# Optimization experiments

Measured on AMD Instinct MI355X. Metric: run time of the kernel, lower is better.

Reference implementation:

```python
import jax, jax.numpy as jnp
import numpy as np
import math

HEAD_SIZE = 128
N_EMBED = 2048
B, T = 4, 4096
TOP_K_RATIO = 0.1


def setup_inputs() -> dict:
    key = jax.random.key(0)
    k1, k2, k3, k4 = jax.random.split(key, 4)
    index = jax.random.normal(k1, (B, T, N_EMBED), dtype=jnp.float32)
    s = 1.0 / math.sqrt(N_EMBED)
    Wq = jax.random.normal(k2, (N_EMBED, HEAD_SIZE), dtype=jnp.float32) * s
    Wk = jax.random.normal(k3, (N_EMBED, HEAD_SIZE), dtype=jnp.float32) * s
    Wv = jax.random.normal(k4, (N_EMBED, HEAD_SIZE), dtype=jnp.float32) * s
    return {"index": index, "Wq": Wq, "Wk": Wk, "Wv": Wv}


def reference(index, Wq, Wk, Wv):
    # memory = index (self-attention case)
    Bv, Tv, _ = index.shape
    top_k = int(TOP_K_RATIO * Tv)  # 409

    q = index @ Wq  # [B, T, D]
    k = index @ Wk
    v = index @ Wv

    q_norms = jnp.linalg.norm(q, axis=-1)  # [B, T]
    _, top_idx = jax.lax.top_k(q_norms, top_k)  # [B, K]

    idx = top_idx[..., None]  # [B, K, 1]
    q_topk = jnp.take_along_axis(q, idx, axis=1)  # [B, K, D]
    k_topk = jnp.take_along_axis(k, idx, axis=1)
    v_topk = jnp.take_along_axis(v, idx, axis=1)

    w = jnp.einsum('bid,bjd->bij', q_topk, k_topk) / math.sqrt(HEAD_SIZE)
    # eval mode: no causal mask (only applied in training), dropout = identity
    w = jax.nn.softmax(w, axis=-1)  # stable softmax (internal max subtraction)
    out_topk = w @ v_topk  # [B, K, D]

    batch_idx = jnp.arange(Bv)[:, None]  # [B, 1]
    output = jnp.zeros((Bv, Tv, HEAD_SIZE), dtype=out_topk.dtype)
    output = output.at[batch_idx, top_idx].add(out_topk)  # scatter_add (indices unique)
    return output
```

## Files before the change

### kernel.cpp

```cpp
#include <hip/hip_runtime.h>
#include <hip/hip_bf16.h>

#define NB 4
#define NT 4096
#define NC 2048
#define ND 128
#define NK 409
#define KPAD 416
#define NM (NB * NK)

typedef __attribute__((ext_vector_type(8))) short short8;
typedef __attribute__((ext_vector_type(4))) float f32x4;

union S8U { short8 v; ushort u[8]; };

__device__ __forceinline__ void split2(float x, ushort& h, ushort& l) {
    union { float f; unsigned u; } a; a.f = x;
    unsigned r = a.u + 0x7FFFu + ((a.u >> 16) & 1u);
    h = (ushort)(r >> 16);
    union { unsigned u; float f; } hb; hb.u = ((unsigned)h) << 16;
    float res = x - hb.f;
    union { float f; unsigned u; } b; b.f = res;
    unsigned r2 = b.u + 0x7FFFu + ((b.u >> 16) & 1u);
    l = (ushort)(r2 >> 16);
}

__device__ __forceinline__ uint4 pack8(const ushort* s) {
    uint4 v;
    v.x = (unsigned)s[0] | ((unsigned)s[1] << 16);
    v.y = (unsigned)s[2] | ((unsigned)s[3] << 16);
    v.z = (unsigned)s[4] | ((unsigned)s[5] << 16);
    v.w = (unsigned)s[6] | ((unsigned)s[7] << 16);
    return v;
}

__device__ __forceinline__ int slotOf(int n, int lq) {
    return n * 4 + ((lq + (n >> 1)) & 3);
}

__device__ __forceinline__ void gll16(const void* g, void* l) {
    __builtin_amdgcn_global_load_lds(
        (const __attribute__((address_space(1))) unsigned*)g,
        (__attribute__((address_space(3))) unsigned*)l, 16, 0, 0);
}

__global__ __launch_bounds__(256) void bconv_tiles(
    const float* __restrict__ W, ushort* __restrict__ Bt)
{
    const int kt = blockIdx.x;
    const int t = threadIdx.x;
    const int n = t & 127;
    const int lq0 = (t >> 7) * 2;
    #pragma unroll
    for (int e = 0; e < 2; ++e) {
        int lq = lq0 + e;
        ushort h[8], l[8];
        #pragma unroll
        for (int j = 0; j < 8; ++j) {
            float x = W[(size_t)(kt * 32 + lq * 8 + j) * ND + n];
            split2(x, h[j], l[j]);
        }
        int slot = slotOf(n, lq);
        *(uint4*)&Bt[((size_t)(kt * 2 + 0) * 512 + slot) * 8] = pack8(h);
        *(uint4*)&Bt[((size_t)(kt * 2 + 1) * 512 + slot) * 8] = pack8(l);
    }
}

__global__ __launch_bounds__(256) void qgemm_v2(
    const float* __restrict__ A, const ushort* __restrict__ Bt,
    float* __restrict__ q1, float* __restrict__ q2)
{
    __shared__ __align__(16) ushort BS[2][2][4096];

    const int tid = threadIdx.x;
    const int w = tid >> 6, lane = tid & 63;
    const int wm = w >> 1, wn = w & 1;
    const int lrow = lane & 15, lq = lane >> 4;
    const int m0 = blockIdx.x * 128;
    const int kb = blockIdx.y * (NC / 2);
    const int kt0 = blockIdx.y * ((NC / 2) / 32);
    const int KITER = (NC / 2) / 32;

    const float* arow[4];
    #pragma unroll
    for (int mi = 0; mi < 4; ++mi)
        arow[mi] = A + (size_t)(m0 + wm * 64 + mi * 16 + lrow) * NC + kb + lq * 8;

    int boff[4];
    #pragma unroll
    for (int ni = 0; ni < 4; ++ni)
        boff[ni] = slotOf(wn * 64 + ni * 16 + lrow, lq) * 8;

    f32x4 acc[4][4];
    #pragma unroll
    for (int i = 0; i < 4; ++i)
        #pragma unroll
        for (int j = 0; j < 4; ++j) acc[i][j] = (f32x4){0.f, 0.f, 0.f, 0.f};

    {
        const ushort* gt = Bt + (size_t)kt0 * 2 * 512 * 8;
        #pragma unroll
        for (int p = 0; p < 2; ++p)
            #pragma unroll
            for (int c2 = 0; c2 < 2; ++c2) {
                int c = 2 * w + c2;
                gll16(gt + ((size_t)p * 512 + c * 64 + lane) * 8,
                      &BS[0][p][(c * 64) * 8]);
            }
    }
    float4 fa[8];
    #pragma unroll
    for (int mi = 0; mi < 4; ++mi) {
        fa[2 * mi + 0] = *(const float4*)(arow[mi] + 0);
        fa[2 * mi + 1] = *(const float4*)(arow[mi] + 4);
    }
    __syncthreads();

    for (int kt = 0; kt < KITER; ++kt) {
        const int buf = kt & 1;
        if (kt + 1 < KITER) {
            const ushort* gt = Bt + (size_t)(kt0 + kt + 1) * 2 * 512 * 8;
            #pragma unroll
            for (int p = 0; p < 2; ++p)
                #pragma unroll
                for (int c2 = 0; c2 < 2; ++c2) {
                    int c = 2 * w + c2;
                    gll16(gt + ((size_t)p * 512 + c * 64 + lane) * 8,
                          &BS[buf ^ 1][p][(c * 64) * 8]);
                }
        }
        short8 ah[4], al[4];
        #pragma unroll
        for (int mi = 0; mi < 4; ++mi) {
            S8U H, L;
            float xs[8] = {fa[2*mi].x, fa[2*mi].y, fa[2*mi].z, fa[2*mi].w,
                           fa[2*mi+1].x, fa[2*mi+1].y, fa[2*mi+1].z, fa[2*mi+1].w};
            #pragma unroll
            for (int j = 0; j < 8; ++j) split2(xs[j], H.u[j], L.u[j]);
            ah[mi] = H.v; al[mi] = L.v;
        }
        if (kt + 1 < KITER) {
            #pragma unroll
            for (int mi = 0; mi < 4; ++mi) {
                fa[2 * mi + 0] = *(const float4*)(arow[mi] + (kt + 1) * 32);
                fa[2 * mi + 1] = *(const float4*)(arow[mi] + (kt + 1) * 32 + 4);
            }
        }
        #pragma unroll
        for (int ni = 0; ni < 4; ++ni) {
            short8 bh = *(const short8*)&BS[buf][0][boff[ni]];
            short8 bl = *(const short8*)&BS[buf][1][boff[ni]];
            #pragma unroll
            for (int mi = 0; mi < 4; ++mi) {
                acc[mi][ni] = __builtin_amdgcn_mfma_f32_16x16x32_bf16(ah[mi], bh, acc[mi][ni], 0, 0, 0);
                acc[mi][ni] = __builtin_amdgcn_mfma_f32_16x16x32_bf16(ah[mi], bl, acc[mi][ni], 0, 0, 0);
                acc[mi][ni] = __builtin_amdgcn_mfma_f32_16x16x32_bf16(al[mi], bh, acc[mi][ni], 0, 0, 0);
            }
        }
        __syncthreads();
    }

    float* __restrict__ qd = blockIdx.y ? q2 : q1;
    #pragma unroll
    for (int ni = 0; ni < 4; ++ni) {
        const int col = wn * 64 + ni * 16 + lrow;
        #pragma unroll
        for (int mi = 0; mi < 4; ++mi)
            #pragma unroll
            for (int r = 0; r < 4; ++r) {
                const int grow = m0 + wm * 64 + mi * 16 + lq * 4 + r;
                qd[(size_t)grow * ND + col] = acc[mi][ni][r];
            }
    }
}

__global__ __launch_bounds__(256) void kvgemm_v2(
    const float* __restrict__ X, const ushort* __restrict__ Bkt,
    const ushort* __restrict__ Bvt, const int* __restrict__ topi,
    float* __restrict__ ktop, float* __restrict__ vtop)
{
    __shared__ __align__(16) ushort BS[2][2][4096];

    const int tid = threadIdx.x;
    const int w = tid >> 6, lane = tid & 63;
    const int wm = w >> 1, wn = w & 1;
    const int lrow = lane & 15, lq = lane >> 4;
    const int m0 = blockIdx.x * 64;
    const int kb = blockIdx.y * (NC / 2);
    const int kt0 = blockIdx.y * ((NC / 2) / 32);
    const ushort* __restrict__ Bt = blockIdx.z ? Bvt : Bkt;
    const int KITER = (NC / 2) / 32;

    const float* arow[2];
    #pragma unroll
    for (int mi = 0; mi < 2; ++mi) {
        int gi = m0 + wm * 32 + mi * 16 + lrow;
        int giC = gi < NM ? gi : NM - 1;
        int b = giC / NK, ii = giC % NK;
        int src = topi[b * KPAD + ii];
        arow[mi] = X + ((size_t)b * NT + src) * NC + kb + lq * 8;
    }
    int boff[4];
    #pragma unroll
    for (int ni = 0; ni < 4; ++ni)
        boff[ni] = slotOf(wn * 64 + ni * 16 + lrow, lq) * 8;

    f32x4 acc[2][4];
    #pragma unroll
    for (int i = 0; i < 2; ++i)
        #pragma unroll
        for (int j = 0; j < 4; ++j) acc[i][j] = (f32x4){0.f, 0.f, 0.f, 0.f};

    {
        const ushort* gt = Bt + (size_t)kt0 * 2 * 512 * 8;
        #pragma unroll
        for (int p = 0; p < 2; ++p)
            #pragma unroll
            for (int c2 = 0; c2 < 2; ++c2) {
                int c = 2 * w + c2;
                gll16(gt + ((size_t)p * 512 + c * 64 + lane) * 8,
                      &BS[0][p][(c * 64) * 8]);
            }
    }
    float4 fa[4];
    #pragma unroll
    for (int mi = 0; mi < 2; ++mi) {
        fa[2 * mi + 0] = *(const float4*)(arow[mi] + 0);
        fa[2 * mi + 1] = *(const float4*)(arow[mi] + 4);
    }
    __syncthreads();

    for (int kt = 0; kt < KITER; ++kt) {
        const int buf = kt & 1;
        if (kt + 1 < KITER) {
            const ushort* gt = Bt + (size_t)(kt0 + kt + 1) * 2 * 512 * 8;
            #pragma unroll
            for (int p = 0; p < 2; ++p)
                #pragma unroll
                for (int c2 = 0; c2 < 2; ++c2) {
                    int c = 2 * w + c2;
                    gll16(gt + ((size_t)p * 512 + c * 64 + lane) * 8,
                          &BS[buf ^ 1][p][(c * 64) * 8]);
                }
        }
        short8 ah[2], al[2];
        #pragma unroll
        for (int mi = 0; mi < 2; ++mi) {
            S8U H, L;
            float xs[8] = {fa[2*mi].x, fa[2*mi].y, fa[2*mi].z, fa[2*mi].w,
                           fa[2*mi+1].x, fa[2*mi+1].y, fa[2*mi+1].z, fa[2*mi+1].w};
            #pragma unroll
            for (int j = 0; j < 8; ++j) split2(xs[j], H.u[j], L.u[j]);
            ah[mi] = H.v; al[mi] = L.v;
        }
        if (kt + 1 < KITER) {
            #pragma unroll
            for (int mi = 0; mi < 2; ++mi) {
                fa[2 * mi + 0] = *(const float4*)(arow[mi] + (kt + 1) * 32);
                fa[2 * mi + 1] = *(const float4*)(arow[mi] + (kt + 1) * 32 + 4);
            }
        }
        #pragma unroll
        for (int ni = 0; ni < 4; ++ni) {
            short8 bh = *(const short8*)&BS[buf][0][boff[ni]];
            short8 bl = *(const short8*)&BS[buf][1][boff[ni]];
            #pragma unroll
            for (int mi = 0; mi < 2; ++mi) {
                acc[mi][ni] = __builtin_amdgcn_mfma_f32_16x16x32_bf16(ah[mi], bh, acc[mi][ni], 0, 0, 0);
                acc[mi][ni] = __builtin_amdgcn_mfma_f32_16x16x32_bf16(ah[mi], bl, acc[mi][ni], 0, 0, 0);
                acc[mi][ni] = __builtin_amdgcn_mfma_f32_16x16x32_bf16(al[mi], bh, acc[mi][ni], 0, 0, 0);
            }
        }
        __syncthreads();
    }

    float* __restrict__ dst = blockIdx.z ? vtop : ktop;
    #pragma unroll
    for (int ni = 0; ni < 4; ++ni) {
        const int col = wn * 64 + ni * 16 + lrow;
        #pragma unroll
        for (int mi = 0; mi < 2; ++mi)
            #pragma unroll
            for (int r = 0; r < 4; ++r) {
                const int grow = m0 + wm * 32 + mi * 16 + lq * 4 + r;
                if (grow < NM)
                    atomicAdd(&dst[(size_t)grow * ND + col], acc[mi][ni][r]);
            }
    }
}

__global__ __launch_bounds__(256) void qnorm_kernel(
    float* __restrict__ q1, const float* __restrict__ q2, float* __restrict__ qn)
{
    const int wv = (blockIdx.x * 256 + threadIdx.x) >> 6;
    const int lane = threadIdx.x & 63;
    float* r1 = q1 + (size_t)wv * ND;
    const float* r2 = q2 + (size_t)wv * ND;
    float a = r1[lane] + r2[lane];
    float b = r1[lane + 64] + r2[lane + 64];
    r1[lane] = a;
    r1[lane + 64] = b;
    float s = a * a + b * b;
    #pragma unroll
    for (int off = 32; off > 0; off >>= 1) s += __shfl_xor(s, off);
    if (lane == 0) qn[wv] = sqrtf(s);
}

__global__ __launch_bounds__(256) void topk_kernel(
    const float* __restrict__ qn, int* __restrict__ topi, int* __restrict__ cnt)
{
    __shared__ int rs[4][64];
    const int b = blockIdx.y;
    const int is = threadIdx.x & 63;
    const int i = blockIdx.x * 64 + is;
    const int chunk = threadIdx.x >> 6;
    const float vi = qn[(size_t)b * NT + i];
    const float4* qv = (const float4*)(qn + (size_t)b * NT + chunk * 1024);
    int rank = 0;
    #pragma unroll 4
    for (int j4 = 0; j4 < 256; ++j4) {
        float4 v = qv[j4];
        int j = chunk * 1024 + j4 * 4;
        rank += (v.x > vi || (v.x == vi && (j + 0) < i)) ? 1 : 0;
        rank += (v.y > vi || (v.y == vi && (j + 1) < i)) ? 1 : 0;
        rank += (v.z > vi || (v.z == vi && (j + 2) < i)) ? 1 : 0;
        rank += (v.w > vi || (v.w == vi && (j + 3) < i)) ? 1 : 0;
    }
    rs[chunk][is] = rank;
    __syncthreads();
    if (threadIdx.x < 64) {
        int rk = rs[0][threadIdx.x] + rs[1][threadIdx.x] + rs[2][threadIdx.x] + rs[3][threadIdx.x];
        if (rk < NK) {
            int p = atomicAdd(&cnt[b], 1);
            topi[b * KPAD + p] = blockIdx.x * 64 + threadIdx.x;
        }
    }
}

__global__ __launch_bounds__(256) void attn_kernel(
    const float* __restrict__ q, const float* __restrict__ ktop,
    const float* __restrict__ vtop, const int* __restrict__ topi,
    float* __restrict__ out)
{
    __shared__ float qs[ND];
    __shared__ float ss[KPAD];
    __shared__ float red[256];
    __shared__ float pv[2][ND];
    const int bi = blockIdx.x;
    const int b = bi / NK, i = bi % NK;
    const int t = threadIdx.x;
    const int row = topi[b * KPAD + i];
    if (t < ND) qs[t] = q[((size_t)b * NT + row) * ND + t];
    __syncthreads();

    const float scale = 0.08838834764831844f;
    float mymax = -1e30f;
    #pragma unroll
    for (int rep = 0; rep < 2; ++rep) {
        int j = t + rep * 256;
        if (j < NK) {
            const float4* kr = (const float4*)(ktop + ((size_t)b * NK + j) * ND);
            const float4* q4 = (const float4*)qs;
            float s = 0.f;
            #pragma unroll
            for (int dd = 0; dd < 32; ++dd) {
                float4 a = q4[dd], kv = kr[dd];
                s += a.x * kv.x + a.y * kv.y + a.z * kv.z + a.w * kv.w;
            }
            s *= scale;
            ss[j] = s;
            mymax = fmaxf(mymax, s);
        }
    }
    red[t] = mymax;
    __syncthreads();
    for (int off = 128; off > 0; off >>= 1) {
        if (t < off) red[t] = fmaxf(red[t], red[t + off]);
        __syncthreads();
    }
    const float mx = red[0];
    __syncthreads();

    float mysum = 0.f;
    #pragma unroll
    for (int rep = 0; rep < 2; ++rep) {
        int j = t + rep * 256;
        if (j < NK) {
            float p = __expf(ss[j] - mx);
            ss[j] = p;
            mysum += p;
        }
    }
    red[t] = mysum;
    __syncthreads();
    for (int off = 128; off > 0; off >>= 1) {
        if (t < off) red[t] += red[t + off];
        __syncthreads();
    }
    const float inv = 1.f / red[0];

    const int col = t & (ND - 1), half = t >> 7;
    float o = 0.f;
    #pragma unroll 4
    for (int j = half; j < NK; j += 2)
        o = fmaf(ss[j], vtop[((size_t)b * NK + j) * ND + col], o);
    pv[half][col] = o;
    __syncthreads();
    if (t < ND)
        out[((size_t)b * NT + row) * ND + t] = (pv[0][t] + pv[1][t]) * inv;
}

extern "C" void kernel_launch(void* const* d_in, const int* in_sizes, int n_in,
                              void* d_out, int out_size, void* d_ws, size_t ws_size,
                              hipStream_t stream)
{
    const float* index = (const float*)d_in[0];
    const float* Wq = (const float*)d_in[1];
    const float* Wk = (const float*)d_in[2];
    const float* Wv = (const float*)d_in[3];
    float* out = (float*)d_out;

    char* ws = (char*)d_ws;
    float*  q1   = (float*)(ws);
    float*  qn   = (float*)(ws + 8388608);
    int*    topi = (int*)  (ws + 8454144);
    int*    cnt  = (int*)  (ws + 8462336);
    ushort* Bqt  = (ushort*)(ws + 8462592);
    float*  ktop = (float*)(ws + 8462592);
    float*  vtop = (float*)(ws + 9300224);

    float*  q2  = (float*)d_out;
    ushort* Bkt = (ushort*)d_out;
    ushort* Bvt = (ushort*)((char*)d_out + 1048576);

    hipMemsetAsync(cnt, 0, NB * sizeof(int), stream);

    bconv_tiles<<<dim3(64), dim3(256), 0, stream>>>(Wq, Bqt);
    qgemm_v2<<<dim3(NB * NT / 128, 2), dim3(256), 0, stream>>>(index, Bqt, q1, q2);
    qnorm_kernel<<<dim3(NB * NT / 4), dim3(256), 0, stream>>>(q1, q2, qn);
    topk_kernel<<<dim3(NT / 64, NB), dim3(256), 0, stream>>>(qn, topi, cnt);
    bconv_tiles<<<dim3(64), dim3(256), 0, stream>>>(Wk, Bkt);
    bconv_tiles<<<dim3(64), dim3(256), 0, stream>>>(Wv, Bvt);
    hipMemsetAsync(ktop, 0, 2 * 837632, stream);
    kvgemm_v2<<<dim3((NM + 63) / 64, 2, 2), dim3(256), 0, stream>>>(
        index, Bkt, Bvt, topi, ktop, vtop);
    hipMemsetAsync(d_out, 0, (size_t)out_size * sizeof(float), stream);
    attn_kernel<<<dim3(NM), dim3(256), 0, stream>>>(q1, ktop, vtop, topi, out);
}
```

Before: 392.2 us.

## Raise split-K to 8 for Q and KV GEMMs using atomic accumulation

The Q projection GEMM now splits the reduction dimension eight ways instead of two, and its partial results are accumulated with atomicAdd into one zeroed buffer instead of two separate buffers that qnorm used to sum. The KV GEMM split also goes from two to eight, and both kernels get a min-blocks-per-CU launch bound. The aim is many more blocks for better CU occupancy on the large Q GEMM. The cost is more fp32 atomic traffic, an extra memset of the Q buffer, and results whose summation order is no longer deterministic.

```diff
diff --git a/kernel.cpp b/kernel.cpp
--- a/kernel.cpp
+++ b/kernel.cpp
@@ -66,9 +66,10 @@
     }
 }
 
-__global__ __launch_bounds__(256) void qgemm_v2(
+#define QSPLIT 8
+__global__ __launch_bounds__(256, 4) void qgemm_v3(
     const float* __restrict__ A, const ushort* __restrict__ Bt,
-    float* __restrict__ q1, float* __restrict__ q2)
+    float* __restrict__ q)
 {
     __shared__ __align__(16) ushort BS[2][2][4096];
 
@@ -77,9 +78,9 @@
     const int wm = w >> 1, wn = w & 1;
     const int lrow = lane & 15, lq = lane >> 4;
     const int m0 = blockIdx.x * 128;
-    const int kb = blockIdx.y * (NC / 2);
-    const int kt0 = blockIdx.y * ((NC / 2) / 32);
-    const int KITER = (NC / 2) / 32;
+    const int kb = blockIdx.y * (NC / QSPLIT);
+    const int kt0 = blockIdx.y * ((NC / QSPLIT) / 32);
+    const int KITER = (NC / QSPLIT) / 32;
 
     const float* arow[4];
     #pragma unroll
@@ -160,7 +161,6 @@
         __syncthreads();
     }
 
-    float* __restrict__ qd = blockIdx.y ? q2 : q1;
     #pragma unroll
     for (int ni = 0; ni < 4; ++ni) {
         const int col = wn * 64 + ni * 16 + lrow;
@@ -169,12 +169,13 @@
             #pragma unroll
             for (int r = 0; r < 4; ++r) {
                 const int grow = m0 + wm * 64 + mi * 16 + lq * 4 + r;
-                qd[(size_t)grow * ND + col] = acc[mi][ni][r];
-            }
-    }
-}
-
-__global__ __launch_bounds__(256) void kvgemm_v2(
+                atomicAdd(&q[(size_t)grow * ND + col], acc[mi][ni][r]);
+            }
+    }
+}
+
+#define KVSPLIT 8
+__global__ __launch_bounds__(256, 4) void kvgemm_v3(
     const float* __restrict__ X, const ushort* __restrict__ Bkt,
     const ushort* __restrict__ Bvt, const int* __restrict__ topi,
     float* __restrict__ ktop, float* __restrict__ vtop)
@@ -186,10 +187,10 @@
     const int wm = w >> 1, wn = w & 1;
     const int lrow = lane & 15, lq = lane >> 4;
     const int m0 = blockIdx.x * 64;
-    const int kb = blockIdx.y * (NC / 2);
-    const int kt0 = blockIdx.y * ((NC / 2) / 32);
+    const int kb = blockIdx.y * (NC / KVSPLIT);
+    const int kt0 = blockIdx.y * ((NC / KVSPLIT) / 32);
     const ushort* __restrict__ Bt = blockIdx.z ? Bvt : Bkt;
-    const int KITER = (NC / 2) / 32;
+    const int KITER = (NC / KVSPLIT) / 32;
 
     const float* arow[2];
     #pragma unroll
@@ -290,16 +291,13 @@
 }
 
 __global__ __launch_bounds__(256) void qnorm_kernel(
-    float* __restrict__ q1, const float* __restrict__ q2, float* __restrict__ qn)
+    const float* __restrict__ q, float* __restrict__ qn)
 {
     const int wv = (blockIdx.x * 256 + threadIdx.x) >> 6;
     const int lane = threadIdx.x & 63;
-    float* r1 = q1 + (size_t)wv * ND;
-    const float* r2 = q2 + (size_t)wv * ND;
-    float a = r1[lane] + r2[lane];
-    float b = r1[lane + 64] + r2[lane + 64];
-    r1[lane] = a;
-    r1[lane + 64] = b;
+    const float* r1 = q + (size_t)wv * ND;
+    float a = r1[lane];
+    float b = r1[lane + 64];
     float s = a * a + b * b;
     #pragma unroll
     for (int off = 32; off > 0; off >>= 1) s += __shfl_xor(s, off);
@@ -429,20 +427,20 @@
     float*  ktop = (float*)(ws + 8462592);
     float*  vtop = (float*)(ws + 9300224);
 
-    float*  q2  = (float*)d_out;
     ushort* Bkt = (ushort*)d_out;
     ushort* Bvt = (ushort*)((char*)d_out + 1048576);
 
     hipMemsetAsync(cnt, 0, NB * sizeof(int), stream);
+    hipMemsetAsync(q1, 0, 8388608, stream);
 
     bconv_tiles<<<dim3(64), dim3(256), 0, stream>>>(Wq, Bqt);
-    qgemm_v2<<<dim3(NB * NT / 128, 2), dim3(256), 0, stream>>>(index, Bqt, q1, q2);
-    qnorm_kernel<<<dim3(NB * NT / 4), dim3(256), 0, stream>>>(q1, q2, qn);
+    qgemm_v3<<<dim3(NB * NT / 128, QSPLIT), dim3(256), 0, stream>>>(index, Bqt, q1);
+    qnorm_kernel<<<dim3(NB * NT / 4), dim3(256), 0, stream>>>(q1, qn);
     topk_kernel<<<dim3(NT / 64, NB), dim3(256), 0, stream>>>(qn, topi, cnt);
     bconv_tiles<<<dim3(64), dim3(256), 0, stream>>>(Wk, Bkt);
     bconv_tiles<<<dim3(64), dim3(256), 0, stream>>>(Wv, Bvt);
     hipMemsetAsync(ktop, 0, 2 * 837632, stream);
-    kvgemm_v2<<<dim3((NM + 63) / 64, 2, 2), dim3(256), 0, stream>>>(
+    kvgemm_v3<<<dim3((NM + 63) / 64, KVSPLIT, 2), dim3(256), 0, stream>>>(
         index, Bkt, Bvt, topi, ktop, vtop);
     hipMemsetAsync(d_out, 0, (size_t)out_size * sizeof(float), stream);
     attn_kernel<<<dim3(NM), dim3(256), 0, stream>>>(q1, ktop, vtop, topi, out);
```

Result: slower. 546.0 us (+39.2%).

## Drop LDS staging in Q/KV GEMMs, load B fragments to registers, raise KV split-K

Applied to the files above, without the earlier changes.

Rewrites the Q and KV projection GEMMs so each wave owns 16 rows across all 128 columns and loads the pre-split bf16 weight fragments straight from global memory into double-buffered registers. This removes shared-memory staging and the per-iteration barriers. The Q tile shrinks to 64 rows, and the KV GEMM split-K grows from 2 to 8 slices to give the small gathered GEMM more blocks. In exchange, weight fragments are re-read from global/L2 by every wave and register pressure rises, and the larger split adds more atomic traffic into ktop/vtop.

```diff
diff --git a/kernel.cpp b/kernel.cpp
--- a/kernel.cpp
+++ b/kernel.cpp
@@ -38,12 +38,6 @@
     return n * 4 + ((lq + (n >> 1)) & 3);
 }
 
-__device__ __forceinline__ void gll16(const void* g, void* l) {
-    __builtin_amdgcn_global_load_lds(
-        (const __attribute__((address_space(1))) unsigned*)g,
-        (__attribute__((address_space(3))) unsigned*)l, 16, 0, 0);
-}
-
 __global__ __launch_bounds__(256) void bconv_tiles(
     const float* __restrict__ W, ushort* __restrict__ Bt)
 {
@@ -66,226 +60,174 @@
     }
 }
 
-__global__ __launch_bounds__(256) void qgemm_v2(
+#define QSPLIT 2
+__global__ __launch_bounds__(256) void qgemm_v5(
     const float* __restrict__ A, const ushort* __restrict__ Bt,
     float* __restrict__ q1, float* __restrict__ q2)
 {
-    __shared__ __align__(16) ushort BS[2][2][4096];
-
     const int tid = threadIdx.x;
     const int w = tid >> 6, lane = tid & 63;
-    const int wm = w >> 1, wn = w & 1;
     const int lrow = lane & 15, lq = lane >> 4;
-    const int m0 = blockIdx.x * 128;
-    const int kb = blockIdx.y * (NC / 2);
-    const int kt0 = blockIdx.y * ((NC / 2) / 32);
-    const int KITER = (NC / 2) / 32;
-
-    const float* arow[4];
-    #pragma unroll
-    for (int mi = 0; mi < 4; ++mi)
-        arow[mi] = A + (size_t)(m0 + wm * 64 + mi * 16 + lrow) * NC + kb + lq * 8;
-
-    int boff[4];
-    #pragma unroll
-    for (int ni = 0; ni < 4; ++ni)
-        boff[ni] = slotOf(wn * 64 + ni * 16 + lrow, lq) * 8;
-
-    f32x4 acc[4][4];
-    #pragma unroll
-    for (int i = 0; i < 4; ++i)
-        #pragma unroll
-        for (int j = 0; j < 4; ++j) acc[i][j] = (f32x4){0.f, 0.f, 0.f, 0.f};
-
+    const int m0 = blockIdx.x * 64;
+    const int KITER = (NC / QSPLIT) / 32;
+    const int kt0 = blockIdx.y * KITER;
+    const int kb = blockIdx.y * (NC / QSPLIT);
+
+    const float* arow = A + (size_t)(m0 + w * 16 + lrow) * NC + kb + lq * 8;
+
+    int boff[8];
+    #pragma unroll
+    for (int ni = 0; ni < 8; ++ni)
+        boff[ni] = slotOf(ni * 16 + lrow, lq) * 8;
+
+    f32x4 acc[8];
+    #pragma unroll
+    for (int i = 0; i < 8; ++i) acc[i] = (f32x4){0.f, 0.f, 0.f, 0.f};
+
+    short8 bhA[8], blA[8], bhB[8], blB[8];
     {
-        const ushort* gt = Bt + (size_t)kt0 * 2 * 512 * 8;
-        #pragma unroll
-        for (int p = 0; p < 2; ++p)
-            #pragma unroll
-            for (int c2 = 0; c2 < 2; ++c2) {
-                int c = 2 * w + c2;
-                gll16(gt + ((size_t)p * 512 + c * 64 + lane) * 8,
-                      &BS[0][p][(c * 64) * 8]);
-            }
-    }
-    float4 fa[8];
-    #pragma unroll
-    for (int mi = 0; mi < 4; ++mi) {
-        fa[2 * mi + 0] = *(const float4*)(arow[mi] + 0);
-        fa[2 * mi + 1] = *(const float4*)(arow[mi] + 4);
-    }
-    __syncthreads();
-
-    for (int kt = 0; kt < KITER; ++kt) {
-        const int buf = kt & 1;
-        if (kt + 1 < KITER) {
-            const ushort* gt = Bt + (size_t)(kt0 + kt + 1) * 2 * 512 * 8;
-            #pragma unroll
-            for (int p = 0; p < 2; ++p)
-                #pragma unroll
-                for (int c2 = 0; c2 < 2; ++c2) {
-                    int c = 2 * w + c2;
-                    gll16(gt + ((size_t)p * 512 + c * 64 + lane) * 8,
-                          &BS[buf ^ 1][p][(c * 64) * 8]);
-                }
-        }
-        short8 ah[4], al[4];
-        #pragma unroll
-        for (int mi = 0; mi < 4; ++mi) {
-            S8U H, L;
-            float xs[8] = {fa[2*mi].x, fa[2*mi].y, fa[2*mi].z, fa[2*mi].w,
-                           fa[2*mi+1].x, fa[2*mi+1].y, fa[2*mi+1].z, fa[2*mi+1].w};
-            #pragma unroll
-            for (int j = 0; j < 8; ++j) split2(xs[j], H.u[j], L.u[j]);
-            ah[mi] = H.v; al[mi] = L.v;
-        }
-        if (kt + 1 < KITER) {
-            #pragma unroll
-            for (int mi = 0; mi < 4; ++mi) {
-                fa[2 * mi + 0] = *(const float4*)(arow[mi] + (kt + 1) * 32);
-                fa[2 * mi + 1] = *(const float4*)(arow[mi] + (kt + 1) * 32 + 4);
-            }
-        }
-        #pragma unroll
-        for (int ni = 0; ni < 4; ++ni) {
-            short8 bh = *(const short8*)&BS[buf][0][boff[ni]];
-            short8 bl = *(const short8*)&BS[buf][1][boff[ni]];
-            #pragma unroll
-            for (int mi = 0; mi < 4; ++mi) {
-                acc[mi][ni] = __builtin_amdgcn_mfma_f32_16x16x32_bf16(ah[mi], bh, acc[mi][ni], 0, 0, 0);
-                acc[mi][ni] = __builtin_amdgcn_mfma_f32_16x16x32_bf16(ah[mi], bl, acc[mi][ni], 0, 0, 0);
-                acc[mi][ni] = __builtin_amdgcn_mfma_f32_16x16x32_bf16(al[mi], bh, acc[mi][ni], 0, 0, 0);
-            }
-        }
-        __syncthreads();
-    }
+        const ushort* gb = Bt + (size_t)kt0 * 8192;
+        #pragma unroll
+        for (int ni = 0; ni < 8; ++ni) {
+            bhA[ni] = *(const short8*)(gb + boff[ni]);
+            blA[ni] = *(const short8*)(gb + 4096 + boff[ni]);
+        }
+    }
+    float4 fa0 = *(const float4*)(arow + 0);
+    float4 fa1 = *(const float4*)(arow + 4);
+
+#define QSTEP(BHC, BLC, BHN, BLN, KT)                                         \
+    {                                                                         \
+        short8 ah, al;                                                        \
+        {                                                                     \
+            S8U H, L;                                                         \
+            float xs[8] = {fa0.x, fa0.y, fa0.z, fa0.w,                        \
+                           fa1.x, fa1.y, fa1.z, fa1.w};                       \
+            _Pragma("unroll")                                                 \
+            for (int j = 0; j < 8; ++j) split2(xs[j], H.u[j], L.u[j]);        \
+            ah = H.v; al = L.v;                                               \
+        }                                                                     \
+        const int ktn = ((KT) + 1 < KITER) ? (KT) + 1 : (KT);                 \
+        const ushort* gbn = Bt + (size_t)(kt0 + ktn) * 8192;                  \
+        _Pragma("unroll")                                                     \
+        for (int ni = 0; ni < 8; ++ni) {                                      \
+            BHN[ni] = *(const short8*)(gbn + boff[ni]);                       \
+            BLN[ni] = *(const short8*)(gbn + 4096 + boff[ni]);                \
+        }                                                                     \
+        fa0 = *(const float4*)(arow + ktn * 32);                              \
+        fa1 = *(const float4*)(arow + ktn * 32 + 4);                          \
+        _Pragma("unroll")                                                     \
+        for (int ni = 0; ni < 8; ++ni) {                                      \
+            acc[ni] = __builtin_amdgcn_mfma_f32_16x16x32_bf16(ah, BHC[ni], acc[ni], 0, 0, 0); \
+            acc[ni] = __builtin_amdgcn_mfma_f32_16x16x32_bf16(ah, BLC[ni], acc[ni], 0, 0, 0); \
+            acc[ni] = __builtin_amdgcn_mfma_f32_16x16x32_bf16(al, BHC[ni], acc[ni], 0, 0, 0); \
+        }                                                                     \
+    }
+
+    for (int kt = 0; kt < KITER; kt += 2) {
+        QSTEP(bhA, blA, bhB, blB, kt);
+        QSTEP(bhB, blB, bhA, blA, kt + 1);
+    }
+#undef QSTEP
 
     float* __restrict__ qd = blockIdx.y ? q2 : q1;
     #pragma unroll
-    for (int ni = 0; ni < 4; ++ni) {
-        const int col = wn * 64 + ni * 16 + lrow;
-        #pragma unroll
-        for (int mi = 0; mi < 4; ++mi)
-            #pragma unroll
-            for (int r = 0; r < 4; ++r) {
-                const int grow = m0 + wm * 64 + mi * 16 + lq * 4 + r;
-                qd[(size_t)grow * ND + col] = acc[mi][ni][r];
-            }
-    }
-}
-
-__global__ __launch_bounds__(256) void kvgemm_v2(
+    for (int ni = 0; ni < 8; ++ni) {
+        const int col = ni * 16 + lrow;
+        #pragma unroll
+        for (int r = 0; r < 4; ++r) {
+            const int grow = m0 + w * 16 + lq * 4 + r;
+            qd[(size_t)grow * ND + col] = acc[ni][r];
+        }
+    }
+}
+
+#define KVSPLIT 8
+__global__ __launch_bounds__(256) void kvgemm_v5(
     const float* __restrict__ X, const ushort* __restrict__ Bkt,
     const ushort* __restrict__ Bvt, const int* __restrict__ topi,
     float* __restrict__ ktop, float* __restrict__ vtop)
 {
-    __shared__ __align__(16) ushort BS[2][2][4096];
-
     const int tid = threadIdx.x;
     const int w = tid >> 6, lane = tid & 63;
-    const int wm = w >> 1, wn = w & 1;
     const int lrow = lane & 15, lq = lane >> 4;
     const int m0 = blockIdx.x * 64;
-    const int kb = blockIdx.y * (NC / 2);
-    const int kt0 = blockIdx.y * ((NC / 2) / 32);
+    const int KITER = (NC / KVSPLIT) / 32;
+    const int kt0 = blockIdx.y * KITER;
+    const int kb = blockIdx.y * (NC / KVSPLIT);
     const ushort* __restrict__ Bt = blockIdx.z ? Bvt : Bkt;
-    const int KITER = (NC / 2) / 32;
-
-    const float* arow[2];
-    #pragma unroll
-    for (int mi = 0; mi < 2; ++mi) {
-        int gi = m0 + wm * 32 + mi * 16 + lrow;
-        int giC = gi < NM ? gi : NM - 1;
-        int b = giC / NK, ii = giC % NK;
-        int src = topi[b * KPAD + ii];
-        arow[mi] = X + ((size_t)b * NT + src) * NC + kb + lq * 8;
-    }
-    int boff[4];
-    #pragma unroll
-    for (int ni = 0; ni < 4; ++ni)
-        boff[ni] = slotOf(wn * 64 + ni * 16 + lrow, lq) * 8;
-
-    f32x4 acc[2][4];
-    #pragma unroll
-    for (int i = 0; i < 2; ++i)
-        #pragma unroll
-        for (int j = 0; j < 4; ++j) acc[i][j] = (f32x4){0.f, 0.f, 0.f, 0.f};
-
+
+    const int gi = m0 + w * 16 + lrow;
+    const int giC = gi < NM ? gi : NM - 1;
+    const int b = giC / NK, ii = giC % NK;
+    const int src = topi[b * KPAD + ii];
+    const float* arow = X + ((size_t)b * NT + src) * NC + kb + lq * 8;
+
+    int boff[8];
+    #pragma unroll
+    for (int ni = 0; ni < 8; ++ni)
+        boff[ni] = slotOf(ni * 16 + lrow, lq) * 8;
+
+    f32x4 acc[8];
+    #pragma unroll
+    for (int i = 0; i < 8; ++i) acc[i] = (f32x4){0.f, 0.f, 0.f, 0.f};
+
+    short8 bhA[8], blA[8], bhB[8], blB[8];
     {
-        const ushort* gt = Bt + (size_t)kt0 * 2 * 512 * 8;
-        #pragma unroll
-        for (int p = 0; p < 2; ++p)
-            #pragma unroll
-            for (int c2 = 0; c2 < 2; ++c2) {
-                int c = 2 * w + c2;
-                gll16(gt + ((size_t)p * 512 + c * 64 + lane) * 8,
-                      &BS[0][p][(c * 64) * 8]);
-            }
-    }
-    float4 fa[4];
-    #pragma unroll
-    for (int mi = 0; mi < 2; ++mi) {
-        fa[2 * mi + 0] = *(const float4*)(arow[mi] + 0);
-        fa[2 * mi + 1] = *(const float4*)(arow[mi] + 4);
-    }
-    __syncthreads();
-
-    for (int kt = 0; kt < KITER; ++kt) {
-        const int buf = kt & 1;
-        if (kt + 1 < KITER) {
-            const ushort* gt = Bt + (size_t)(kt0 + kt + 1) * 2 * 512 * 8;
-            #pragma unroll
-            for (int p = 0; p < 2; ++p)
-                #pragma unroll
-                for (int c2 = 0; c2 < 2; ++c2) {
-                    int c = 2 * w + c2;
-                    gll16(gt + ((size_t)p * 512 + c * 64 + lane) * 8,
-                          &BS[buf ^ 1][p][(c * 64) * 8]);
-                }
-        }
-        short8 ah[2], al[2];
-        #pragma unroll
-        for (int mi = 0; mi < 2; ++mi) {
-            S8U H, L;
-            float xs[8] = {fa[2*mi].x, fa[2*mi].y, fa[2*mi].z, fa[2*mi].w,
-                           fa[2*mi+1].x, fa[2*mi+1].y, fa[2*mi+1].z, fa[2*mi+1].w};
-            #pragma unroll
-            for (int j = 0; j < 8; ++j) split2(xs[j], H.u[j], L.u[j]);
-            ah[mi] = H.v; al[mi] = L.v;
-        }
-        if (kt + 1 < KITER) {
-            #pragma unroll
-            for (int mi = 0; mi < 2; ++mi) {
-                fa[2 * mi + 0] = *(const float4*)(arow[mi] + (kt + 1) * 32);
-                fa[2 * mi + 1] = *(const float4*)(arow[mi] + (kt + 1) * 32 + 4);
-            }
-        }
-        #pragma unroll
-        for (int ni = 0; ni < 4; ++ni) {
-            short8 bh = *(const short8*)&BS[buf][0][boff[ni]];
-            short8 bl = *(const short8*)&BS[buf][1][boff[ni]];
-            #pragma unroll
-            for (int mi = 0; mi < 2; ++mi) {
-                acc[mi][ni] = __builtin_amdgcn_mfma_f32_16x16x32_bf16(ah[mi], bh, acc[mi][ni], 0, 0, 0);
-                acc[mi][ni] = __builtin_amdgcn_mfma_f32_16x16x32_bf16(ah[mi], bl, acc[mi][ni], 0, 0, 0);
-                acc[mi][ni] = __builtin_amdgcn_mfma_f32_16x16x32_bf16(al[mi], bh, acc[mi][ni], 0, 0, 0);
-            }
-        }
-        __syncthreads();
-    }
+        const ushort* gb = Bt + (size_t)kt0 * 8192;
+        #pragma unroll
+        for (int ni = 0; ni < 8; ++ni) {
+            bhA[ni] = *(const short8*)(gb + boff[ni]);
+            blA[ni] = *(const short8*)(gb + 4096 + boff[ni]);
+        }
+    }
+    float4 fa0 = *(const float4*)(arow + 0);
+    float4 fa1 = *(const float4*)(arow + 4);
+
+#define QSTEP(BHC, BLC, BHN, BLN, KT)                                         \
+    {                                                                         \
+        short8 ah, al;                                                        \
+        {                                                                     \
+            S8U H, L;                                                         \
+            float xs[8] = {fa0.x, fa0.y, fa0.z, fa0.w,                        \
+                           fa1.x, fa1.y, fa1.z, fa1.w};                       \
+            _Pragma("unroll")                                                 \
+            for (int j = 0; j < 8; ++j) split2(xs[j], H.u[j], L.u[j]);        \
+            ah = H.v; al = L.v;                                               \
+        }                                                                     \
+        const int ktn = ((KT) + 1 < KITER) ? (KT) + 1 : (KT);                 \
+        const ushort* gbn = Bt + (size_t)(kt0 + ktn) * 8192;                  \
+        _Pragma("unroll")                                                     \
+        for (int ni = 0; ni < 8; ++ni) {                                      \
+            BHN[ni] = *(const short8*)(gbn + boff[ni]);                       \
+            BLN[ni] = *(const short8*)(gbn + 4096 + boff[ni]);                \
+        }                                                                     \
+        fa0 = *(const float4*)(arow + ktn * 32);                              \
+        fa1 = *(const float4*)(arow + ktn * 32 + 4);                          \
+        _Pragma("unroll")                                                     \
+        for (int ni = 0; ni < 8; ++ni) {                                      \
+            acc[ni] = __builtin_amdgcn_mfma_f32_16x16x32_bf16(ah, BHC[ni], acc[ni], 0, 0, 0); \
+            acc[ni] = __builtin_amdgcn_mfma_f32_16x16x32_bf16(ah, BLC[ni], acc[ni], 0, 0, 0); \
+            acc[ni] = __builtin_amdgcn_mfma_f32_16x16x32_bf16(al, BHC[ni], acc[ni], 0, 0, 0); \
+        }                                                                     \
+    }
+
+    for (int kt = 0; kt < KITER; kt += 2) {
+        QSTEP(bhA, blA, bhB, blB, kt);
+        QSTEP(bhB, blB, bhA, blA, kt + 1);
+    }
+#undef QSTEP
 
     float* __restrict__ dst = blockIdx.z ? vtop : ktop;
     #pragma unroll
-    for (int ni = 0; ni < 4; ++ni) {
-        const int col = wn * 64 + ni * 16 + lrow;
-        #pragma unroll
-        for (int mi = 0; mi < 2; ++mi)
-            #pragma unroll
-            for (int r = 0; r < 4; ++r) {
-                const int grow = m0 + wm * 32 + mi * 16 + lq * 4 + r;
-                if (grow < NM)
-                    atomicAdd(&dst[(size_t)grow * ND + col], acc[mi][ni][r]);
-            }
+    for (int ni = 0; ni < 8; ++ni) {
+        const int col = ni * 16 + lrow;
+        #pragma unroll
+        for (int r = 0; r < 4; ++r) {
+            const int grow = m0 + w * 16 + lq * 4 + r;
+            if (grow < NM)
+                atomicAdd(&dst[(size_t)grow * ND + col], acc[ni][r]);
+        }
     }
 }
 
@@ -436,13 +378,13 @@
     hipMemsetAsync(cnt, 0, NB * sizeof(int), stream);
 
     bconv_tiles<<<dim3(64), dim3(256), 0, stream>>>(Wq, Bqt);
-    qgemm_v2<<<dim3(NB * NT / 128, 2), dim3(256), 0, stream>>>(index, Bqt, q1, q2);
+    qgemm_v5<<<dim3(NB * NT / 64, QSPLIT), dim3(256), 0, stream>>>(index, Bqt, q1, q2);
     qnorm_kernel<<<dim3(NB * NT / 4), dim3(256), 0, stream>>>(q1, q2, qn);
     topk_kernel<<<dim3(NT / 64, NB), dim3(256), 0, stream>>>(qn, topi, cnt);
     bconv_tiles<<<dim3(64), dim3(256), 0, stream>>>(Wk, Bkt);
     bconv_tiles<<<dim3(64), dim3(256), 0, stream>>>(Wv, Bvt);
     hipMemsetAsync(ktop, 0, 2 * 837632, stream);
-    kvgemm_v2<<<dim3((NM + 63) / 64, 2, 2), dim3(256), 0, stream>>>(
+    kvgemm_v5<<<dim3((NM + 63) / 64, KVSPLIT, 2), dim3(256), 0, stream>>>(
         index, Bkt, Bvt, topi, ktop, vtop);
     hipMemsetAsync(d_out, 0, (size_t)out_size * sizeof(float), stream);
     attn_kernel<<<dim3(NM), dim3(256), 0, stream>>>(q1, ktop, vtop, topi, out);
```

Result: faster. 370.3 us (-5.6%).
